# Optimization experiments

Measured on AMD Instinct MI355X. Metric: run time of the kernel, lower is better.

The kernel has to match this reference:

```python
import jax, jax.numpy as jnp
from jax import lax
import numpy as np

B, K, H, W = 16, 8, 256, 256


def setup_inputs() -> dict:
    key = jax.random.key(0)
    masks = jax.random.normal(key, (B, K, H, W), dtype=jnp.float32)
    return {"masks": masks}


def _nlccs_loss_one(mask):
    """Per-mask loss. mask: (H, W) float, already rescaled/clamped.

    Replicates cv2.connectedComponentsWithStats (8-connectivity, background is
    a single label regardless of connectivity), sorts components by area, and
    suppresses (zeroes a pmask over) the bounding box of the second-largest
    component, then returns mean(pmask * mask).
    """
    h, w = mask.shape
    S = h * w  # sentinel / background label
    sent = jnp.int32(S)
    fg = lax.stop_gradient(mask) > 0.5  # cv2 threshold (arr > 0.5)
    idx = jnp.arange(S, dtype=jnp.int32).reshape(h, w)
    lab0 = jnp.where(fg, idx, sent)

    def step(lab):
        # 8-connectivity neighbor-min propagation (cv2 default connectivity=8)
        p = jnp.pad(lab, 1, constant_values=S)
        m = lab
        for dy in (-1, 0, 1):
            for dx in (-1, 0, 1):
                if dy == 0 and dx == 0:
                    continue
                m = jnp.minimum(m, p[1 + dy:1 + dy + h, 1 + dx:1 + dx + w])
        lab = jnp.where(fg, m, sent)
        # pointer jumping: lab <- lab[lab] for log-time convergence
        ext = jnp.concatenate([lab.reshape(-1), jnp.array([S], jnp.int32)])
        return jnp.where(fg, ext[lab], sent)

    def cond(c):
        lab, prev = c
        return jnp.any(lab != prev)

    def body(c):
        lab, _ = c
        return step(lab), lab

    lab, _ = lax.while_loop(cond, body, (step(lab0), lab0))

    # per-label areas; background pixels all share label S (like cv2 label 0)
    areas = jnp.zeros(S + 1, jnp.int32).at[lab.reshape(-1)].add(1)
    _, top_idx = lax.top_k(areas, 2)
    second = top_idx[1]  # stats sorted by area -> stats[-2]

    # bounding box of the second-largest component
    sel = lab == second
    rows = jnp.arange(h, dtype=jnp.int32)[:, None]
    cols = jnp.arange(w, dtype=jnp.int32)[None, :]
    h0 = jnp.min(jnp.where(sel, rows, h))
    h1 = jnp.max(jnp.where(sel, rows, -1)) + 1
    w0 = jnp.min(jnp.where(sel, cols, w))
    w1 = jnp.max(jnp.where(sel, cols, -1)) + 1
    inside = (rows >= h0) & (rows < h1) & (cols >= w0) & (cols < w1)
    pmask = 1.0 - inside.astype(mask.dtype)  # pmask[h0:h1, w0:w1] = 0
    return (pmask * mask).mean()


def reference(masks):
    # masks: (b, k, h, w)
    m = jnp.maximum((masks + 1.0) * 0.5, 0.0)  # ((masks+1)/2).clamp(min=0)
    flat = m.reshape(-1, m.shape[-2], m.shape[-1])  # (b*k, h, w)
    losses = jax.vmap(_nlccs_loss_one)(flat)
    return losses.mean()
```

## Files before the change

kernel.cpp:

```cpp
#include <hip/hip_runtime.h>

#define HH 256
#define WW 256
#define SS 65536
#define NM 128
#define TRR 16
#define NT2 16
#define RMX 2048
#define SPT 1024
#define SPM 16384

struct Meta {
  double dsum[NM];
  int h0[NM]; int h1[NM]; int w0[NM]; int w1[NM];
};

__device__ __forceinline__ int find_c(int* L, int x) {
  int p = L[x];
  if (p == x) return x;
  int root = p, q = L[root];
  while (q != root) { root = q; q = L[root]; }
  if (root != p) L[x] = root;
  return root;
}

__device__ void unite(int* L, int a, int b) {
  bool done = false;
  do {
    a = find_c(L, a);
    b = find_c(L, b);
    if (a < b)      { int old = atomicMin(&L[b], a); done = (old == b); b = old; }
    else if (b < a) { int old = atomicMin(&L[a], b); done = (old == a); a = old; }
    else done = true;
  } while (!done);
}

__device__ __forceinline__ int find_halve(int* L, int x) {
  int p = L[x];
  while (p != x) {
    int gp = L[p];
    if (gp == p) return p;
    L[x] = gp;
    x = p; p = gp;
  }
  return x;
}

__device__ __forceinline__ int cid(const unsigned long long* rm,
                                   const int* rpre, int r) {
  int w = r >> 6, b = r & 63;
  return rpre[w] + (int)__popcll(rm[w] & (b ? ((1ull << b) - 1) : 0ull));
}

__device__ __forceinline__ unsigned long long mask_le(int b) {
  return (b == 63) ? ~0ull : ((1ull << (b + 1)) - 1);
}
__device__ __forceinline__ unsigned long long mask_lt(int b) {
  return b ? ((1ull << b) - 1) : 0ull;
}

__global__ __launch_bounds__(512)
void k_local(const float* __restrict__ in, int cb,
             int* __restrict__ gp, int* __restrict__ ga,
             unsigned int* __restrict__ gbb, unsigned short* __restrict__ gl,
             unsigned short* __restrict__ gbrow, int* __restrict__ gnr,
             double* __restrict__ tdsum, unsigned int* __restrict__ tbb,
             int* __restrict__ gfg0) {
  __shared__ unsigned long long sfgw[TRR][4];
  __shared__ unsigned char sfgc[TRR][32];
  __shared__ unsigned long long srs[TRR][4];
  __shared__ int wpre64[64];
  __shared__ int snr;
  __shared__ int sspan[RMX];
  __shared__ int suf[RMX];
  __shared__ unsigned long long rootm[32];
  __shared__ int rpre[32];
  __shared__ int sA[SPT], sW0[SPT], sW1[SPT], sH0[SPT], sH1[SPT];
  __shared__ double sred[8];
  __shared__ int sbb[4][8];

  int q = blockIdx.x, lm = q >> 4, tile = q & 15;
  int tid = threadIdx.x, lane = tid & 63, wv = tid >> 6;
  int gm = cb + lm, R0 = tile << 4;

  int r1 = tid >> 5, cs = tid & 31;
  const float4* src =
      (const float4*)(in + ((size_t)gm << 16) + ((R0 + r1) << 8) + (cs << 3));
  double dsum = 0.0;
  unsigned int fgb = 0;
  for (int k = 0; k < 2; k++) {
    float4 v = src[k];
    float m0 = fmaxf((v.x + 1.0f) * 0.5f, 0.0f);
    float m1 = fmaxf((v.y + 1.0f) * 0.5f, 0.0f);
    float m2 = fmaxf((v.z + 1.0f) * 0.5f, 0.0f);
    float m3 = fmaxf((v.w + 1.0f) * 0.5f, 0.0f);
    dsum += (double)m0 + (double)m1 + (double)m2 + (double)m3;
    fgb |= ((m0 > 0.5f) ? 1u : 0u) << (4 * k);
    fgb |= ((m1 > 0.5f) ? 1u : 0u) << (4 * k + 1);
    fgb |= ((m2 > 0.5f) ? 1u : 0u) << (4 * k + 2);
    fgb |= ((m3 > 0.5f) ? 1u : 0u) << (4 * k + 3);
  }
  sfgc[r1][cs] = (unsigned char)fgb;
  __syncthreads();
  if (tid < 64) {
    int row = tid >> 2, w = tid & 3;
    const unsigned char* pc = &sfgc[row][w << 3];
    unsigned long long wd = 0;
    for (int i = 0; i < 8; i++) wd |= ((unsigned long long)pc[i]) << (i << 3);
    sfgw[row][w] = wd;
  }
  __syncthreads();

  if (tid < 64) {
    int row = tid >> 2, w = tid & 3;
    unsigned long long W = sfgw[row][w];
    unsigned long long carry = (w > 0) ? (sfgw[row][w - 1] >> 63) : 0ull;
    unsigned long long rs = W & ~((W << 1) | carry);
    srs[row][w] = rs;
    int cnt = (int)__popcll(rs);
    int sa = cnt;
    for (int off = 1; off < 64; off <<= 1) {
      int t = __shfl_up(sa, off);
      if (tid >= off) sa += t;
    }
    wpre64[tid] = sa - cnt;
    if (tid == 63) snr = sa;
    int id = sa - cnt;
    unsigned long long bits = rs;
    while (bits) {
      int a = (int)__ffsll(bits) - 1;
      bits &= bits - 1;
      int A = (w << 6) + a;
      unsigned long long inv = ~(W >> a);
      int len = inv ? ((int)__ffsll(inv) - 1) : (64 - a);
      if (len == 64 - a) {
        for (int w2 = w + 1; w2 < 4; w2++) {
          unsigned long long iv2 = ~sfgw[row][w2];
          int t = iv2 ? ((int)__ffsll(iv2) - 1) : 64;
          len += t;
          if (t < 64) break;
        }
      }
      sspan[id] = (row << 16) | (A << 8) | (A + len - 1);
      suf[id] = id;
      id++;
    }
  } else {
    for (int s = tid - 64; s < SPT; s += 448) {
      sA[s] = 0; sW0[s] = WW; sW1[s] = -1; sH0[s] = TRR; sH1[s] = -1;
    }
  }
  __syncthreads();

  int nr = snr;

  for (int i = tid; i < nr; i += 512) {
    int sp = sspan[i];
    int row = sp >> 16, a = (sp >> 8) & 255, b = sp & 255;
    if (row == 0) continue;
    int lo = max(a - 1, 0), hi = min(b + 1, 255);
    const unsigned long long* Wp = sfgw[row - 1];
    const unsigned long long* Rp = srs[row - 1];
    int prebase = (row - 1) << 2;
    int lw = lo >> 6, lb = lo & 63;
    if (((Wp[lw] >> lb) & 1) && !((Rp[lw] >> lb) & 1)) {
      int j = wpre64[prebase + lw] + (int)__popcll(Rp[lw] & mask_le(lb)) - 1;
      unite(suf, i, j);
    }
    for (int w = lw; w <= (hi >> 6); w++) {
      unsigned long long m = Rp[w];
      if (w == lw) m &= ~mask_lt(lb);
      if (w == (hi >> 6)) m &= mask_le(hi & 63);
      int base2 = wpre64[prebase + w];
      while (m) {
        int bb = (int)__ffsll(m) - 1;
        m &= m - 1;
        int j = base2 + (int)__popcll(Rp[w] & mask_lt(bb));
        unite(suf, i, j);
      }
    }
  }
  __syncthreads();

  for (int j = 0; j < 4; j++) {
    int i = tid + (j << 9);
    unsigned long long bal = __ballot(i < nr && suf[i] == i);
    if (lane == 0) rootm[wv + (j << 3)] = bal;
  }
  __syncthreads();
  if (tid < 32) {
    int pc = (int)__popcll(rootm[tid]);
    int sa = pc;
    for (int off = 1; off < 32; off <<= 1) {
      int t = __shfl_up(sa, off);
      if (tid >= off) sa += t;
    }
    rpre[tid] = sa - pc;
  }
  __syncthreads();

  for (int i = tid; i < nr; i += 512) {
    int root = find_halve(suf, i);
    int id = cid(rootm, rpre, root);
    int sp = sspan[i];
    int row = sp >> 16, a = (sp >> 8) & 255, b = sp & 255;
    atomicAdd(&sA[id], b - a + 1);
    if (a < sW0[id]) atomicMin(&sW0[id], a);
    if (b > sW1[id]) atomicMax(&sW1[id], b);
    if (row < sH0[id]) atomicMin(&sH0[id], row);
    if (row > sH1[id]) atomicMax(&sH1[id], row);
  }
  __syncthreads();

  int nc = rpre[31] + (int)__popcll(rootm[31]);
  for (int i = tid; i < nr; i += 512) {
    if (suf[i] == i) {
      int id = cid(rootm, rpre, i);
      int gid = (lm << 14) + (tile << 10) + id;
      int sp = sspan[i];
      gp[gid] = gid;
      ga[gid] = sA[id];
      gl[gid] = (unsigned short)((tile << 12) + ((sp >> 16) << 8) +
                                 ((sp >> 8) & 255));
      gbb[gid] = ((unsigned)(R0 + sH0[id]) << 24) | ((unsigned)sW0[id] << 16)
               | ((unsigned)(R0 + sH1[id]) << 8) | (unsigned)sW1[id];
    }
  }
  {
    int c = tid & 255, topbot = tid >> 8;
    int brow = topbot ? (TRR - 1) : 0;
    unsigned short val = 0xFFFF;
    if ((sfgw[brow][c >> 6] >> (c & 63)) & 1) {
      int w = c >> 6, bb = c & 63;
      int id = wpre64[(brow << 2) + w] +
               (int)__popcll(srs[brow][w] & mask_le(bb)) - 1;
      int root = find_halve(suf, id);
      val = (unsigned short)((tile << 10) + cid(rootm, rpre, root));
    }
    gbrow[(q << 9) + (topbot ? 256 : 0) + c] = val;
  }
  if (tid == 0) gnr[q] = nc;

  int c = tid & 255, half = (tid >> 8) << 3;
  int bh0r = TRR, bh1r = -1;
  bool anybg = false;
  for (int row = half; row < half + 8; row++) {
    if (!((sfgw[row][c >> 6] >> (c & 63)) & 1)) {
      anybg = true;
      bh0r = min(bh0r, row); bh1r = max(bh1r, row);
    }
  }
  int bw0r = anybg ? c : WW, bw1r = anybg ? c : -1;
  for (int off = 32; off > 0; off >>= 1) {
    bw0r = min(bw0r, __shfl_down(bw0r, off));
    bw1r = max(bw1r, __shfl_down(bw1r, off));
    bh0r = min(bh0r, __shfl_down(bh0r, off));
    bh1r = max(bh1r, __shfl_down(bh1r, off));
  }
  if (lane == 0) { sbb[0][wv] = bw0r; sbb[1][wv] = bw1r;
                   sbb[2][wv] = bh0r; sbb[3][wv] = bh1r; }
  for (int off = 32; off > 0; off >>= 1) dsum += __shfl_down(dsum, off);
  if (lane == 0) sred[wv] = dsum;
  __syncthreads();
  if (tid == 0) {
    int a0 = sbb[0][0], a1 = sbb[1][0], a2 = sbb[2][0], a3 = sbb[3][0];
    for (int i = 1; i < 8; i++) {
      a0 = min(a0, sbb[0][i]); a1 = max(a1, sbb[1][i]);
      a2 = min(a2, sbb[2][i]); a3 = max(a3, sbb[3][i]);
    }
    unsigned pack = (a1 >= 0)
        ? (((unsigned)(R0 + a2) << 24) | ((unsigned)a0 << 16) |
           ((unsigned)(R0 + a3) << 8) | (unsigned)a1)
        : 0xFFFF0000u;
    tbb[q] = pack;
    double t = 0.0;
    for (int i = 0; i < 8; i++) t += sred[i];
    tdsum[q] = t;
    if (tile == 0) gfg0[lm] = (int)(sfgw[0][0] & 1ull);
  }
}

__global__ void k_seam(int* __restrict__ gp,
                       const unsigned short* __restrict__ gbrow) {
  int b = blockIdx.x;
  int lm = b / 15, s = b % 15;
  int tb = lm << 4;
  int sbase = lm << 14;
  const unsigned short* up = gbrow + ((tb + s) << 9) + 256;
  const unsigned short* lo = gbrow + ((tb + s + 1) << 9);
  int c = threadIdx.x;
  unsigned short v16 = lo[c];
  if (v16 == 0xFFFF) return;
  int v = sbase + v16;
  bool wfg = (c > 0) && (lo[c - 1] != 0xFFFF);
  unsigned short n16 = up[c];
  if (!wfg) {
    if (n16 != 0xFFFF) unite(gp, v, sbase + n16);
    else if (c > 0 && up[c - 1] != 0xFFFF) unite(gp, v, sbase + up[c - 1]);
  }
  if (n16 == 0xFFFF && c < 255 && up[c + 1] != 0xFFFF)
    unite(gp, v, sbase + up[c + 1]);
}

__global__ void k_push(int* __restrict__ gp, int* __restrict__ ga,
                       const int* __restrict__ gnr) {
  int q = blockIdx.x;
  int lm = q >> 4;
  int sbase = lm << 14;
  int nc = gnr[q];
  int tid = threadIdx.x, lane = tid & 63;
  for (int t = 0; t < 4; t++) {
    int slot = (t << 8) + tid;
    int r = -1, a = 0;
    if (slot < nc) {
      int gid = sbase + ((q & 15) << 10) + slot;
      int rr = find_c(gp, gid);
      if (rr != gid) { r = rr; a = ga[gid]; }
    }
    bool pend = (r >= 0);
    while (__any(pend)) {
      unsigned long long mk = __ballot(pend);
      int srcl = (int)__ffsll(mk) - 1;
      int lead = __shfl(r, srcl);
      bool mine = pend && (r == lead);
      int v = mine ? a : 0;
      for (int off = 32; off > 0; off >>= 1) v += __shfl_down(v, off);
      int tot = __shfl(v, 0);
      if (lane == srcl) atomicAdd(&ga[lead], tot);
      pend = pend && !mine;
    }
  }
}

__global__ void k_top2p(const int* __restrict__ gp, const int* __restrict__ ga,
                        const unsigned short* __restrict__ gl,
                        const int* __restrict__ gnr,
                        unsigned long long* __restrict__ tt1,
                        unsigned long long* __restrict__ tt2,
                        int* __restrict__ tfs) {
  int q = blockIdx.x;
  int lm = q >> 4, tile = q & 15;
  int sbase = lm << 14;
  int nc = gnr[q];
  int tid = threadIdx.x, lane = tid & 63, wv = tid >> 6;
  unsigned long long t1 = 0, t2 = 0;
  int fsum = 0;
  for (int sl = tid; sl < nc; sl += 256) {
    int s = (tile << 10) + sl;
    int gid = sbase + s;
    if (gp[gid] == gid) {
      int a = ga[gid];
      int lab = gl[gid];
      fsum += a;
      unsigned long long key = ((unsigned long long)a << 37)
                             | ((unsigned long long)(SS - lab) << 20)
                             | (unsigned)s;
      if (key > t1) { t2 = t1; t1 = key; }
      else if (key > t2) t2 = key;
    }
  }
  for (int off = 32; off > 0; off >>= 1) {
    unsigned long long o1 = __shfl_down(t1, off), o2 = __shfl_down(t2, off);
    if (o1 > t1) { t2 = (t1 > o2) ? t1 : o2; t1 = o1; }
    else if (o1 > t2) t2 = o1;
    fsum += __shfl_down(fsum, off);
  }
  __shared__ unsigned long long s1[4], s2[4];
  __shared__ int sf[4];
  if (lane == 0) { s1[wv] = t1; s2[wv] = t2; sf[wv] = fsum; }
  __syncthreads();
  if (tid == 0) {
    for (int i = 1; i < 4; i++) {
      unsigned long long o1 = s1[i], o2 = s2[i];
      if (o1 > t1) { t2 = (t1 > o2) ? t1 : o2; t1 = o1; }
      else if (o1 > t2) t2 = o1;
      fsum += sf[i];
    }
    tt1[q] = t1; tt2[q] = t2; tfs[q] = fsum;
  }
}

__global__ __launch_bounds__(64)
void k_mask(const double* __restrict__ tdsum,
            const unsigned int* __restrict__ tbb,
            const unsigned long long* __restrict__ tt1,
            const unsigned long long* __restrict__ tt2,
            const int* __restrict__ tfs, const int* __restrict__ gfg0,
            int* __restrict__ psec, Meta* __restrict__ mt, int c0) {
  int lm = blockIdx.x, gm = c0 + lm;
  int tid = threadIdx.x;
  int tb = lm << 4;
  double d = 0.0;
  int h0 = 255, w0 = 255, h1 = 0, w1 = 0;
  unsigned long long t1 = 0, t2 = 0;
  int fsum = 0;
  if (tid < 16) {
    d = tdsum[tb + tid];
    unsigned bb = tbb[tb + tid];
    h0 = (int)(bb >> 24); w0 = (int)((bb >> 16) & 255);
    h1 = (int)((bb >> 8) & 255); w1 = (int)(bb & 255);
    t1 = tt1[tb + tid]; t2 = tt2[tb + tid]; fsum = tfs[tb + tid];
  }
  for (int off = 8; off > 0; off >>= 1) {
    d += __shfl_down(d, off);
    h0 = min(h0, __shfl_down(h0, off));
    w0 = min(w0, __shfl_down(w0, off));
    h1 = max(h1, __shfl_down(h1, off));
    w1 = max(w1, __shfl_down(w1, off));
    unsigned long long o1 = __shfl_down(t1, off), o2 = __shfl_down(t2, off);
    if (o1 > t1) { t2 = (t1 > o2) ? t1 : o2; t1 = o1; }
    else if (o1 > t2) t2 = o1;
    fsum += __shfl_down(fsum, off);
  }
  if (tid == 0) {
    mt->dsum[gm] = d;
    unsigned long long bg = ((unsigned long long)(SS - fsum)) << 37;
    int zl = gfg0[lm] ? 1 : 0;
    unsigned long long zk = ((unsigned long long)(SS - zl)) << 20;
    if (bg > t1) { t2 = t1; t1 = bg; } else if (bg > t2) t2 = bg;
    if (zk > t1) { t2 = t1; t1 = zk; } else if (zk > t2) t2 = zk;
    if (t2 == bg) {
      psec[lm] = -1;
      mt->h0[gm] = h0; mt->h1[gm] = h1; mt->w0[gm] = w0; mt->w1[gm] = w1;
    } else if (t2 == zk) {
      psec[lm] = -1;
      mt->h0[gm] = 1; mt->h1[gm] = 0; mt->w0[gm] = 1; mt->w1[gm] = 0;
    } else {
      psec[lm] = (lm << 14) + (int)(t2 & 0xFFFFF);
      mt->h0[gm] = HH; mt->h1[gm] = -1; mt->w0[gm] = WW; mt->w1[gm] = -1;
    }
  }
}

__global__ void k_sweep(int* __restrict__ gp,
                        const unsigned int* __restrict__ gbb,
                        const int* __restrict__ gnr,
                        const int* __restrict__ psec,
                        Meta* __restrict__ mt, int c0) {
  int q = blockIdx.x;
  int lm = q >> 4, tile = q & 15;
  int gm = c0 + lm;
  int sec = psec[lm];
  if (sec < 0) return;
  int sbase = lm << 14;
  int nc = gnr[q];
  int tid = threadIdx.x, lane = tid & 63, wv = tid >> 6;
  int h0l = HH, h1l = -1, w0l = WW, w1l = -1;
  for (int sl = tid; sl < nc; sl += 256) {
    int gid = sbase + (tile << 10) + sl;
    if (find_c(gp, gid) == sec) {
      unsigned int bb = gbb[gid];
      h0l = min(h0l, (int)(bb >> 24));
      w0l = min(w0l, (int)((bb >> 16) & 255));
      h1l = max(h1l, (int)((bb >> 8) & 255));
      w1l = max(w1l, (int)(bb & 255));
    }
  }
  for (int off = 32; off > 0; off >>= 1) {
    h0l = min(h0l, __shfl_down(h0l, off));
    w0l = min(w0l, __shfl_down(w0l, off));
    h1l = max(h1l, __shfl_down(h1l, off));
    w1l = max(w1l, __shfl_down(w1l, off));
  }
  __shared__ int r0[4], r1[4], r2[4], r3[4];
  if (lane == 0) { r0[wv] = h0l; r1[wv] = h1l; r2[wv] = w0l; r3[wv] = w1l; }
  __syncthreads();
  if (tid == 0) {
    for (int i = 1; i < 4; i++) {
      r0[0] = min(r0[0], r0[i]); r1[0] = max(r1[0], r1[i]);
      r2[0] = min(r2[0], r2[i]); r3[0] = max(r3[0], r3[i]);
    }
    if (r1[0] >= 0) {
      atomicMin(&mt->h0[gm], r0[0]);
      atomicMax(&mt->h1[gm], r1[0]);
      atomicMin(&mt->w0[gm], r2[0]);
      atomicMax(&mt->w1[gm], r3[0]);
    }
  }
}

__global__ void k_inside(const float* __restrict__ in,
                         const Meta* __restrict__ mt,
                         double* __restrict__ dinsp, int c0) {
  int b = blockIdx.x;
  int lm = b >> 3, seg = b & 7;
  int gm = c0 + lm;
  int h0 = mt->h0[gm], h1 = mt->h1[gm], w0 = mt->w0[gm], w1 = mt->w1[gm];
  double acc = 0.0;
  if (h1 >= h0) {
    int cc = w0 + threadIdx.x;
    if (cc <= w1) {
      const float* base = in + ((size_t)gm << 16);
      for (int rr = h0 + seg; rr <= h1; rr += 8) {
        float x = base[(rr << 8) + cc];
        acc += (double)fmaxf((x + 1.0f) * 0.5f, 0.0f);
      }
    }
  }
  for (int off = 32; off > 0; off >>= 1) acc += __shfl_down(acc, off);
  __shared__ double sd[4];
  int wid = threadIdx.x >> 6, lane = threadIdx.x & 63;
  if (lane == 0) sd[wid] = acc;
  __syncthreads();
  if (threadIdx.x == 0)
    dinsp[(gm << 3) + seg] = sd[0] + sd[1] + sd[2] + sd[3];
}

__global__ void k_final(const Meta* __restrict__ mt,
                        const double* __restrict__ dinsp,
                        float* __restrict__ out) {
  __shared__ double sd[NM];
  int t = threadIdx.x;
  double di = 0.0;
  for (int s = 0; s < 8; s++) di += dinsp[(t << 3) + s];
  sd[t] = (mt->dsum[t] - di) / (double)SS;
  __syncthreads();
  for (int off = 64; off > 0; off >>= 1) {
    if (t < off) sd[t] += sd[t + off];
    __syncthreads();
  }
  if (t == 0) out[0] = (float)(sd[0] / (double)NM);
}

extern "C" void kernel_launch(void* const* d_in, const int* in_sizes, int n_in,
                              void* d_out, int out_size, void* d_ws,
                              size_t ws_size, hipStream_t stream) {
  const float* in = (const float*)d_in[0];
  float* out = (float*)d_out;

  Meta* mt = (Meta*)d_ws;
  const size_t meta_bytes = (sizeof(Meta) + 255) & ~(size_t)255;
  char* base = (char*)d_ws + meta_bytes;
  size_t fixed = (size_t)NM * 8 * sizeof(double);
  size_t avail = (ws_size > meta_bytes + fixed)
                     ? (ws_size - meta_bytes - fixed) : 0;
  const size_t per_mask = (size_t)NT2 * 8 + NT2 * 4 + 4 +
                          (size_t)SPM * (4 + 4 + 4 + 2) +
                          (size_t)NT2 * 512 * 2 + NT2 * 4 +
                          (size_t)NT2 * (8 + 8 + 4) + 4;
  int chunk = (int)(avail / per_mask);
  if (chunk > NM) chunk = NM;
  if (chunk < 1) return;

  char* ptr = base;
  double* dinsp = (double*)ptr;        ptr += fixed;
  double* tdsum = (double*)ptr;        ptr += (size_t)chunk * NT2 * 8;
  unsigned long long* tt1 = (unsigned long long*)ptr;
  ptr += (size_t)chunk * NT2 * 8;
  unsigned long long* tt2 = (unsigned long long*)ptr;
  ptr += (size_t)chunk * NT2 * 8;
  int* gp = (int*)ptr;                 ptr += (size_t)chunk * SPM * 4;
  int* ga = (int*)ptr;                 ptr += (size_t)chunk * SPM * 4;
  unsigned int* gbb = (unsigned int*)ptr;       ptr += (size_t)chunk * SPM * 4;
  unsigned short* gl = (unsigned short*)ptr;    ptr += (size_t)chunk * SPM * 2;
  unsigned short* gbrow = (unsigned short*)ptr; ptr += (size_t)chunk * NT2 * 512 * 2;
  int* gnr = (int*)ptr;                ptr += (size_t)chunk * NT2 * 4;
  unsigned int* tbb = (unsigned int*)ptr;       ptr += (size_t)chunk * NT2 * 4;
  int* tfs = (int*)ptr;                ptr += (size_t)chunk * NT2 * 4;
  int* gfg0 = (int*)ptr;               ptr += (size_t)chunk * 4;
  int* psec = (int*)ptr;

  for (int c0 = 0; c0 < NM; c0 += chunk) {
    int cn = (chunk < NM - c0) ? chunk : (NM - c0);
    k_local<<<cn * NT2, 512, 0, stream>>>(in, c0, gp, ga, gbb, gl, gbrow,
                                          gnr, tdsum, tbb, gfg0);
    k_seam <<<cn * 15, 256, 0, stream>>>(gp, gbrow);
    k_push <<<cn * NT2, 256, 0, stream>>>(gp, ga, gnr);
    k_top2p<<<cn * NT2, 256, 0, stream>>>(gp, ga, gl, gnr, tt1, tt2, tfs);
    k_mask <<<cn, 64, 0, stream>>>(tdsum, tbb, tt1, tt2, tfs, gfg0, psec,
                                   mt, c0);
    k_sweep<<<cn * NT2, 256, 0, stream>>>(gp, gbb, gnr, psec, mt, c0);
    k_inside<<<cn * 8, 256, 0, stream>>>(in, mt, dinsp, c0);
  }
  k_final<<<1, 128, 0, stream>>>(mt, dinsp, out);
}
```

Baseline: 188.1 us.

## Merge bounding boxes into roots during area push, drop sweep kernel

The area-push kernel now also merges each component's packed bounding box into its root, using a wave reduction followed by a CAS loop. The mask kernel can then read the second-largest component's box directly from the root. This removes the separate sweep kernel, which re-ran find on every provisional label and did its own reductions. In exchange, k_push carries extra shuffle reductions and per-root CAS retries under contention, and the psec buffer is removed from the workspace layout.

```diff
diff --git a/kernel.cpp b/kernel.cpp
--- a/kernel.cpp
+++ b/kernel.cpp
@@ -303,6 +303,7 @@
 }
 
 __global__ void k_push(int* __restrict__ gp, int* __restrict__ ga,
+                       unsigned int* __restrict__ gbb,
                        const int* __restrict__ gnr) {
   int q = blockIdx.x;
   int lm = q >> 4;
@@ -312,10 +313,16 @@
   for (int t = 0; t < 4; t++) {
     int slot = (t << 8) + tid;
     int r = -1, a = 0;
+    int h0 = HH, w0 = WW, h1 = -1, w1 = -1;
     if (slot < nc) {
       int gid = sbase + ((q & 15) << 10) + slot;
       int rr = find_c(gp, gid);
-      if (rr != gid) { r = rr; a = ga[gid]; }
+      if (rr != gid) {
+        r = rr; a = ga[gid];
+        unsigned int bb = gbb[gid];
+        h0 = (int)(bb >> 24); w0 = (int)((bb >> 16) & 255);
+        h1 = (int)((bb >> 8) & 255); w1 = (int)(bb & 255);
+      }
     }
     bool pend = (r >= 0);
     while (__any(pend)) {
@@ -323,10 +330,38 @@
       int srcl = (int)__ffsll(mk) - 1;
       int lead = __shfl(r, srcl);
       bool mine = pend && (r == lead);
-      int v = mine ? a : 0;
-      for (int off = 32; off > 0; off >>= 1) v += __shfl_down(v, off);
+      int v  = mine ? a  : 0;
+      int g0 = mine ? h0 : HH;
+      int g1 = mine ? h1 : -1;
+      int g2 = mine ? w0 : WW;
+      int g3 = mine ? w1 : -1;
+      for (int off = 32; off > 0; off >>= 1) {
+        v += __shfl_down(v, off);
+        g0 = min(g0, __shfl_down(g0, off));
+        g1 = max(g1, __shfl_down(g1, off));
+        g2 = min(g2, __shfl_down(g2, off));
+        g3 = max(g3, __shfl_down(g3, off));
+      }
       int tot = __shfl(v, 0);
-      if (lane == srcl) atomicAdd(&ga[lead], tot);
+      int m0 = __shfl(g0, 0), m1 = __shfl(g1, 0);
+      int m2 = __shfl(g2, 0), m3 = __shfl(g3, 0);
+      if (lane == srcl) {
+        atomicAdd(&ga[lead], tot);
+        unsigned int* dst = &gbb[lead];
+        unsigned int old = *dst;
+        while (true) {
+          int oh0 = (int)(old >> 24), ow0 = (int)((old >> 16) & 255);
+          int oh1 = (int)((old >> 8) & 255), ow1 = (int)(old & 255);
+          int nh0 = min(oh0, m0), nw0 = min(ow0, m2);
+          int nh1 = max(oh1, m1), nw1 = max(ow1, m3);
+          unsigned int mrg = ((unsigned)nh0 << 24) | ((unsigned)nw0 << 16) |
+                             ((unsigned)nh1 << 8) | (unsigned)nw1;
+          if (mrg == old) break;
+          unsigned int got = atomicCAS(dst, old, mrg);
+          if (got == old) break;
+          old = got;
+        }
+      }
       pend = pend && !mine;
     }
   }
@@ -386,7 +421,8 @@
             const unsigned long long* __restrict__ tt1,
             const unsigned long long* __restrict__ tt2,
             const int* __restrict__ tfs, const int* __restrict__ gfg0,
-            int* __restrict__ psec, Meta* __restrict__ mt, int c0) {
+            const unsigned int* __restrict__ gbb,
+            Meta* __restrict__ mt, int c0) {
   int lm = blockIdx.x, gm = c0 + lm;
   int tid = threadIdx.x;
   int tb = lm << 4;
@@ -420,61 +456,15 @@
     if (bg > t1) { t2 = t1; t1 = bg; } else if (bg > t2) t2 = bg;
     if (zk > t1) { t2 = t1; t1 = zk; } else if (zk > t2) t2 = zk;
     if (t2 == bg) {
-      psec[lm] = -1;
       mt->h0[gm] = h0; mt->h1[gm] = h1; mt->w0[gm] = w0; mt->w1[gm] = w1;
     } else if (t2 == zk) {
-      psec[lm] = -1;
       mt->h0[gm] = 1; mt->h1[gm] = 0; mt->w0[gm] = 1; mt->w1[gm] = 0;
     } else {
-      psec[lm] = (lm << 14) + (int)(t2 & 0xFFFFF);
-      mt->h0[gm] = HH; mt->h1[gm] = -1; mt->w0[gm] = WW; mt->w1[gm] = -1;
-    }
-  }
-}
-
-__global__ void k_sweep(int* __restrict__ gp,
-                        const unsigned int* __restrict__ gbb,
-                        const int* __restrict__ gnr,
-                        const int* __restrict__ psec,
-                        Meta* __restrict__ mt, int c0) {
-  int q = blockIdx.x;
-  int lm = q >> 4, tile = q & 15;
-  int gm = c0 + lm;
-  int sec = psec[lm];
-  if (sec < 0) return;
-  int sbase = lm << 14;
-  int nc = gnr[q];
-  int tid = threadIdx.x, lane = tid & 63, wv = tid >> 6;
-  int h0l = HH, h1l = -1, w0l = WW, w1l = -1;
-  for (int sl = tid; sl < nc; sl += 256) {
-    int gid = sbase + (tile << 10) + sl;
-    if (find_c(gp, gid) == sec) {
-      unsigned int bb = gbb[gid];
-      h0l = min(h0l, (int)(bb >> 24));
-      w0l = min(w0l, (int)((bb >> 16) & 255));
-      h1l = max(h1l, (int)((bb >> 8) & 255));
-      w1l = max(w1l, (int)(bb & 255));
-    }
-  }
-  for (int off = 32; off > 0; off >>= 1) {
-    h0l = min(h0l, __shfl_down(h0l, off));
-    w0l = min(w0l, __shfl_down(w0l, off));
-    h1l = max(h1l, __shfl_down(h1l, off));
-    w1l = max(w1l, __shfl_down(w1l, off));
-  }
-  __shared__ int r0[4], r1[4], r2[4], r3[4];
-  if (lane == 0) { r0[wv] = h0l; r1[wv] = h1l; r2[wv] = w0l; r3[wv] = w1l; }
-  __syncthreads();
-  if (tid == 0) {
-    for (int i = 1; i < 4; i++) {
-      r0[0] = min(r0[0], r0[i]); r1[0] = max(r1[0], r1[i]);
-      r2[0] = min(r2[0], r2[i]); r3[0] = max(r3[0], r3[i]);
-    }
-    if (r1[0] >= 0) {
-      atomicMin(&mt->h0[gm], r0[0]);
-      atomicMax(&mt->h1[gm], r1[0]);
-      atomicMin(&mt->w0[gm], r2[0]);
-      atomicMax(&mt->w1[gm], r3[0]);
+      unsigned int bb = gbb[(lm << 14) + (int)(t2 & 0xFFFFF)];
+      mt->h0[gm] = (int)(bb >> 24);
+      mt->w0[gm] = (int)((bb >> 16) & 255);
+      mt->h1[gm] = (int)((bb >> 8) & 255);
+      mt->w1[gm] = (int)(bb & 255);
     }
   }
 }
@@ -537,7 +527,7 @@
   const size_t per_mask = (size_t)NT2 * 8 + NT2 * 4 + 4 +
                           (size_t)SPM * (4 + 4 + 4 + 2) +
                           (size_t)NT2 * 512 * 2 + NT2 * 4 +
-                          (size_t)NT2 * (8 + 8 + 4) + 4;
+                          (size_t)NT2 * (8 + 8 + 4);
   int chunk = (int)(avail / per_mask);
   if (chunk > NM) chunk = NM;
   if (chunk < 1) return;
@@ -557,19 +547,17 @@
   int* gnr = (int*)ptr;                ptr += (size_t)chunk * NT2 * 4;
   unsigned int* tbb = (unsigned int*)ptr;       ptr += (size_t)chunk * NT2 * 4;
   int* tfs = (int*)ptr;                ptr += (size_t)chunk * NT2 * 4;
-  int* gfg0 = (int*)ptr;               ptr += (size_t)chunk * 4;
-  int* psec = (int*)ptr;
+  int* gfg0 = (int*)ptr;
 
   for (int c0 = 0; c0 < NM; c0 += chunk) {
     int cn = (chunk < NM - c0) ? chunk : (NM - c0);
     k_local<<<cn * NT2, 512, 0, stream>>>(in, c0, gp, ga, gbb, gl, gbrow,
                                           gnr, tdsum, tbb, gfg0);
     k_seam <<<cn * 15, 256, 0, stream>>>(gp, gbrow);
-    k_push <<<cn * NT2, 256, 0, stream>>>(gp, ga, gnr);
+    k_push <<<cn * NT2, 256, 0, stream>>>(gp, ga, gbb, gnr);
     k_top2p<<<cn * NT2, 256, 0, stream>>>(gp, ga, gl, gnr, tt1, tt2, tfs);
-    k_mask <<<cn, 64, 0, stream>>>(tdsum, tbb, tt1, tt2, tfs, gfg0, psec,
+    k_mask <<<cn, 64, 0, stream>>>(tdsum, tbb, tt1, tt2, tfs, gfg0, gbb,
                                    mt, c0);
-    k_sweep<<<cn * NT2, 256, 0, stream>>>(gp, gbb, gnr, psec, mt, c0);
     k_inside<<<cn * 8, 256, 0, stream>>>(in, mt, dinsp, c0);
   }
   k_final<<<1, 128, 0, stream>>>(mt, dinsp, out);
```

Result: no change. 184.6 us (median of 2 runs) (-1.9%).
